# Kernel optimization log

Measured on AMD Instinct MI355X. Metric: run time of the kernel, lower is better.

## Reference

```python
import jax, jax.numpy as jnp
import numpy as np

U, S, D = 4096, 8192, 32
NUM_REGIONS = 128
GA = 0.1


def setup_inputs() -> dict:
    key = jax.random.key(0)
    k1, k2, k3, k4, k5, k6 = jax.random.split(key, 6)
    user_emb = jax.random.normal(k1, (U, D), dtype=jnp.float32) * 0.01
    item_emb = jax.random.normal(k2, (S, D), dtype=jnp.float32) * 0.01
    train_mask = jax.random.randint(k3, (U, S), 0, 2, dtype=jnp.int32)
    true_qos = jax.random.normal(k4, (U, S), dtype=jnp.float32)
    us_lossweight = jax.random.uniform(k5, (U, S), dtype=jnp.float32)
    region_index = jax.random.randint(k6, (U,), 0, NUM_REGIONS, dtype=jnp.int32)
    return {
        "user_emb": user_emb,
        "item_emb": item_emb,
        "train_mask": train_mask,
        "true_qos": true_qos,
        "us_lossweight": us_lossweight,
        "region_index": region_index,
    }


def _region_loss(user_emb, region_index):
    # per-region sums and counts via a single segment reduction
    sums = jax.ops.segment_sum(user_emb, region_index, num_segments=NUM_REGIONS)  # [R, D]
    counts = jax.ops.segment_sum(jnp.ones((user_emb.shape[0],), dtype=user_emb.dtype),
                                 region_index, num_segments=NUM_REGIONS)  # [R]
    cnt = counts[region_index]                      # [U]
    loo_mean = (sums[region_index] - user_emb) / jnp.maximum(cnt - 1.0, 1.0)[:, None]
    dev = jnp.abs(user_emb - loo_mean)              # [U, D]
    # regions with a single user are skipped in the original loop
    valid = (cnt > 1.0)[:, None]
    return jnp.sum(jnp.where(valid, dev, 0.0))


def reference(user_emb, item_emb, train_mask, true_qos, us_lossweight, region_index):
    pre_qos = (user_emb @ item_emb.T) * train_mask.astype(user_emb.dtype)  # [U, S]
    mse = (pre_qos - true_qos) ** 2
    loss = jnp.sum(us_lossweight * mse)
    regionloss = _region_loss(user_emb, region_index)
    return loss + GA * regionloss
```

## Files before the change

### kernel.cpp

```cpp
#include <hip/hip_runtime.h>

#define U 4096
#define S 8192
#define D 32
#define NUM_REGIONS 128
#define GA 0.1f

#define TU 32
#define TI 256
#define THREADS 256
#define LCAP 256

#define PIN4(v) asm volatile("" : "+v"(v.x), "+v"(v.y), "+v"(v.z), "+v"(v.w))


__global__ __launch_bounds__(THREADS) void fused_kernel(
    const float* __restrict__ user_emb,
    const float* __restrict__ item_emb,
    const int* __restrict__ train_mask,
    const float* __restrict__ true_qos,
    const float* __restrict__ us_lossweight,
    const int* __restrict__ region_index,
    float* __restrict__ loss_accum,
    float* __restrict__ rl_accum) {
    __shared__ float uemb[TU][D];
    __shared__ int   ridx[U];
    __shared__ int   ulist[LCAP];
    __shared__ int   ucnt;
    __shared__ float part[8][D];
    __shared__ float redsum[D];
    __shared__ float wp[THREADS / 64];

    const int ub = blockIdx.x * TU;
    const int sb = blockIdx.y * TI;

    {
        const float4* src = (const float4*)(user_emb + (size_t)ub * D);
        ((float4*)&uemb[0][0])[threadIdx.x] = src[threadIdx.x];
    }

    const int s0 = sb + threadIdx.x;
    float4 ir[8];
    {
        const float4* ip = (const float4*)(item_emb + (size_t)s0 * D);
        #pragma unroll
        for (int k = 0; k < 8; k++) ir[k] = ip[k];
        #pragma unroll
        for (int k = 0; k < 8; k++) PIN4(ir[k]);
    }
    __syncthreads();

    const size_t base0 = (size_t)ub * S + s0;
    int   m_n = train_mask[base0];
    float q_n = true_qos[base0];
    float w_n = us_lossweight[base0];

    float acc = 0.0f;
    #pragma unroll 1
    for (int uu = 0; uu < TU; uu++) {
        int   m = m_n;
        float q = q_n;
        float w = w_n;
        if (uu + 1 < TU) {
            const size_t nb = base0 + (size_t)(uu + 1) * S;
            m_n = train_mask[nb];
            q_n = true_qos[nb];
            w_n = us_lossweight[nb];
        }

        float d0 = 0.0f;
        const float4* ur = (const float4*)&uemb[uu][0];
        #pragma unroll
        for (int k = 0; k < 8; k++) {
            float4 uv = ur[k];
            d0 += uv.x * ir[k].x + uv.y * ir[k].y + uv.z * ir[k].z + uv.w * ir[k].w;
        }
        float p = d0 * (float)m;
        float e = p - q;
        acc += w * e * e;
    }

    #pragma unroll
    for (int off = 32; off > 0; off >>= 1) acc += __shfl_down(acc, off, 64);
    {
        int lane = threadIdx.x & 63, wid = threadIdx.x >> 6;
        if (lane == 0) wp[wid] = acc;
        __syncthreads();
        if (threadIdx.x == 0) {
            float t = 0.0f;
            #pragma unroll
            for (int i = 0; i < THREADS / 64; i++) t += wp[i];
            atomicAdd(loss_accum, t);
        }
    }

    if (blockIdx.y != 0) return;
    const int r = blockIdx.x;

    if (threadIdx.x == 0) ucnt = 0;
    #pragma unroll
    for (int i = 0; i < U / 4 / 256; i++)
        ((int4*)ridx)[threadIdx.x + i * 256] =
            ((const int4*)region_index)[threadIdx.x + i * 256];
    __syncthreads();

    for (int u = threadIdx.x; u < U; u += 256) {
        if (ridx[u] == r) {
            int p = atomicAdd(&ucnt, 1);
            if (p < LCAP) ulist[p] = u;
        }
    }
    __syncthreads();

    const int n = min(ucnt, LCAP);
    const int d = threadIdx.x & (D - 1);
    const int w8 = threadIdx.x >> 5;

    float psum = 0.0f;
    for (int i = w8; i < n; i += 8)
        psum += user_emb[ulist[i] * D + d];
    part[w8][d] = psum;
    __syncthreads();
    if (w8 == 0) {
        float sum = 0.0f;
        #pragma unroll
        for (int i = 0; i < 8; i++) sum += part[i][d];
        redsum[d] = sum;
    }
    __syncthreads();

    float racc = 0.0f;
    if (n > 1) {
        const float inv = 1.0f / (float)(n - 1);
        const float sd = redsum[d];
        for (int i = w8; i < n; i += 8) {
            float e = user_emb[ulist[i] * D + d];
            racc += fabsf(e - (sd - e) * inv);
        }
    }

    #pragma unroll
    for (int off = 32; off > 0; off >>= 1) racc += __shfl_down(racc, off, 64);
    {
        int lane = threadIdx.x & 63, wid = threadIdx.x >> 6;
        if (lane == 0) wp[wid] = racc;
        __syncthreads();
        if (threadIdx.x == 0) {
            float t = 0.0f;
            #pragma unroll
            for (int i = 0; i < THREADS / 64; i++) t += wp[i];
            atomicAdd(rl_accum, t);
        }
    }
}

__global__ void finalize_kernel(const float* __restrict__ loss_acc,
                                const float* __restrict__ rl_acc,
                                float* __restrict__ out) {
    out[0] = loss_acc[0] + GA * rl_acc[0];
}

extern "C" void kernel_launch(void* const* d_in, const int* in_sizes, int n_in,
                              void* d_out, int out_size, void* d_ws, size_t ws_size,
                              hipStream_t stream) {
    const float* user_emb      = (const float*)d_in[0];
    const float* item_emb      = (const float*)d_in[1];
    const int*   train_mask    = (const int*)d_in[2];
    const float* true_qos      = (const float*)d_in[3];
    const float* us_lossweight = (const float*)d_in[4];
    const int*   region_index  = (const int*)d_in[5];
    float* out = (float*)d_out;

    float* ws       = (float*)d_ws;
    float* loss_acc = ws;
    float* rl_acc   = ws + 1;
    hipMemsetAsync(d_ws, 0, 2 * sizeof(float), stream);

    dim3 grid(U / TU, S / TI);
    fused_kernel<<<grid, THREADS, 0, stream>>>(
        user_emb, item_emb, train_mask, true_qos, us_lossweight, region_index,
        loss_acc, rl_acc);

    finalize_kernel<<<1, 1, 0, stream>>>(loss_acc, rl_acc, out);
}
```

Baseline: 383.7 us.

## Batch eight user rows per iteration and stream item embeddings from global

The main loop now loads mask, qos and weight for eight user rows at once and computes eight dot products per pass. Item embedding float4s are re-read from global memory inside the loop instead of being pinned in registers for the whole block. The region pass reads region_index straight from global memory, dropping the 16KB shared staging array. The goal is more memory-level parallelism on the streamed UxS inputs and lower shared-memory and register use for higher occupancy, at the cost of repeated item loads that rely on cache hits.

```diff
diff --git a/kernel.cpp b/kernel.cpp
--- a/kernel.cpp
+++ b/kernel.cpp
@@ -8,10 +8,9 @@
 
 #define TU 32
 #define TI 256
+#define UG 8
 #define THREADS 256
 #define LCAP 256
-
-#define PIN4(v) asm volatile("" : "+v"(v.x), "+v"(v.y), "+v"(v.z), "+v"(v.w))
 
 
 __global__ __launch_bounds__(THREADS) void fused_kernel(
@@ -24,7 +23,6 @@
     float* __restrict__ loss_accum,
     float* __restrict__ rl_accum) {
     __shared__ float uemb[TU][D];
-    __shared__ int   ridx[U];
     __shared__ int   ulist[LCAP];
     __shared__ int   ucnt;
     __shared__ float part[8][D];
@@ -38,46 +36,43 @@
         const float4* src = (const float4*)(user_emb + (size_t)ub * D);
         ((float4*)&uemb[0][0])[threadIdx.x] = src[threadIdx.x];
     }
+    __syncthreads();
 
     const int s0 = sb + threadIdx.x;
-    float4 ir[8];
-    {
-        const float4* ip = (const float4*)(item_emb + (size_t)s0 * D);
-        #pragma unroll
-        for (int k = 0; k < 8; k++) ir[k] = ip[k];
-        #pragma unroll
-        for (int k = 0; k < 8; k++) PIN4(ir[k]);
-    }
-    __syncthreads();
-
-    const size_t base0 = (size_t)ub * S + s0;
-    int   m_n = train_mask[base0];
-    float q_n = true_qos[base0];
-    float w_n = us_lossweight[base0];
+    const float4* ip = (const float4*)(item_emb + (size_t)s0 * D);
 
     float acc = 0.0f;
     #pragma unroll 1
-    for (int uu = 0; uu < TU; uu++) {
-        int   m = m_n;
-        float q = q_n;
-        float w = w_n;
-        if (uu + 1 < TU) {
-            const size_t nb = base0 + (size_t)(uu + 1) * S;
-            m_n = train_mask[nb];
-            q_n = true_qos[nb];
-            w_n = us_lossweight[nb];
+    for (int g = 0; g < TU; g += UG) {
+        int   m[UG]; float q[UG], w[UG];
+        #pragma unroll
+        for (int j = 0; j < UG; j++) {
+            const size_t b = (size_t)(ub + g + j) * S + s0;
+            m[j] = train_mask[b];
+            q[j] = true_qos[b];
+            w[j] = us_lossweight[b];
         }
 
-        float d0 = 0.0f;
-        const float4* ur = (const float4*)&uemb[uu][0];
+        float dsum[UG];
+        #pragma unroll
+        for (int j = 0; j < UG; j++) dsum[j] = 0.0f;
+
         #pragma unroll
         for (int k = 0; k < 8; k++) {
-            float4 uv = ur[k];
-            d0 += uv.x * ir[k].x + uv.y * ir[k].y + uv.z * ir[k].z + uv.w * ir[k].w;
+            float4 iv = ip[k];
+            #pragma unroll
+            for (int j = 0; j < UG; j++) {
+                float4 uv = *(const float4*)&uemb[g + j][k * 4];
+                dsum[j] += uv.x * iv.x + uv.y * iv.y + uv.z * iv.z + uv.w * iv.w;
+            }
         }
-        float p = d0 * (float)m;
-        float e = p - q;
-        acc += w * e * e;
+
+        #pragma unroll
+        for (int j = 0; j < UG; j++) {
+            float p = dsum[j] * (float)m[j];
+            float e = p - q[j];
+            acc += w[j] * e * e;
+        }
     }
 
     #pragma unroll
@@ -97,15 +92,12 @@
     if (blockIdx.y != 0) return;
     const int r = blockIdx.x;
 
+    __syncthreads();
     if (threadIdx.x == 0) ucnt = 0;
-    #pragma unroll
-    for (int i = 0; i < U / 4 / 256; i++)
-        ((int4*)ridx)[threadIdx.x + i * 256] =
-            ((const int4*)region_index)[threadIdx.x + i * 256];
     __syncthreads();
 
     for (int u = threadIdx.x; u < U; u += 256) {
-        if (ridx[u] == r) {
+        if (region_index[u] == r) {
             int p = atomicAdd(&ucnt, 1);
             if (p < LCAP) ulist[p] = u;
         }
```

Result: faster. 375.4 us (-2.2%).
